# Kernel optimization log

Hardware: AMD Instinct MI355X
Metric: run time of the kernel (lower is better)

The kernel has to match this reference:

```python
import jax, jax.numpy as jnp
import numpy as np

B, S, D, UNITS = 32, 4096, 512, 512


def setup_inputs() -> dict:
    key = jax.random.key(0)
    ks = jax.random.split(key, 8)
    scale = 0.05
    return {
        "query": jax.random.normal(ks[0], (B, D), dtype=jnp.float32),
        "values": jax.random.normal(ks[1], (B, S, D), dtype=jnp.float32),
        "W1": jax.random.normal(ks[2], (D, UNITS), dtype=jnp.float32) * scale,
        "b1": jnp.zeros((UNITS,), dtype=jnp.float32),
        "W2": jax.random.normal(ks[3], (D, UNITS), dtype=jnp.float32) * scale,
        "b2": jnp.zeros((UNITS,), dtype=jnp.float32),
        "V": jax.random.normal(ks[4], (UNITS, 1), dtype=jnp.float32) * scale,
        "bv": jnp.zeros((1,), dtype=jnp.float32),
    }


def reference(query, values, W1, b1, W2, b2, V, bv):
    # values: [B, S, D], query: [B, D]
    proj_v = jnp.einsum("bsd,du->bsu", values, W1) + b1          # [B, S, U]
    proj_q = (query @ W2 + b2)[:, None, :]                        # [B, 1, U]
    score = jnp.tanh(proj_v + proj_q) @ V + bv                    # [B, S, 1]
    attention_weights = jax.nn.softmax(score, axis=1)             # [B, S, 1]
    context_vector = jnp.sum(attention_weights * values, axis=1)  # [B, D]
    return (context_vector, attention_weights)
```

## Files before the change

### kernel.cpp

```cpp
#include <hip/hip_runtime.h>

#define NB 32
#define NS 4096
#define ND 512
#define NU 512

typedef __attribute__((ext_vector_type(8))) __bf16 bf16x8;
typedef __attribute__((ext_vector_type(8))) short short8;
typedef __attribute__((ext_vector_type(4))) float f32x4;

union Cvt8 { __bf16 h[8]; short8 s8; };

__device__ __forceinline__ float fast_tanh(float x) {
  float e = __expf(2.0f * x);
  return 1.0f - __fdividef(2.0f, e + 1.0f);
}

__global__ void pack_w1_kernel(const float* __restrict__ W1, __bf16* __restrict__ W1f) {
  int idx = blockIdx.x * 256 + threadIdx.x;
  int l  = idx & 63;
  int ct = (idx >> 6) & 31;
  int ks = idx >> 11;
  int col   = ct * 16 + (l & 15);
  int kbase = ks * 32 + (l >> 4) * 8;
  Cvt8 u;
#pragma unroll
  for (int j = 0; j < 8; ++j) u.h[j] = (__bf16)W1[(size_t)(kbase + j) * NU + col];
  *reinterpret_cast<short8*>(W1f + (size_t)idx * 8) = u.s8;
}

__global__ void proj_query_kernel(const float* __restrict__ query, const float* __restrict__ W2,
                                  const float* __restrict__ b2, const float* __restrict__ b1,
                                  float* __restrict__ pq) {
  int b = blockIdx.y;
  int u = blockIdx.x * 256 + threadIdx.x;
  const float* q = query + (size_t)b * ND;
  float acc = b2[u] + b1[u];
  for (int k = 0; k < ND; ++k) acc += q[k] * W2[(size_t)k * NU + u];
  pq[(size_t)b * NU + u] = acc;
}

__global__ __launch_bounds__(512, 4)
void score_kernel(const float* __restrict__ values, const __bf16* __restrict__ W1f,
                  const float* __restrict__ pq, const float* __restrict__ V,
                  float* __restrict__ scoreW) {
  __shared__ __align__(16) char ldsb[67584];
  float* sbuf = (float*)(ldsb + 65536);

  int bid = blockIdx.x;
  int b = bid >> 6;
  int s0 = (bid & 63) * 64;
  int tid = threadIdx.x;
  int l = tid & 63;
  int w = tid >> 6;
  int lane_col = l & 15;
  int lane_k8  = l >> 4;

  float pqv[4], Vv[4];
#pragma unroll
  for (int nb = 0; nb < 2; ++nb)
#pragma unroll
    for (int cf = 0; cf < 2; ++cf) {
      int col = nb * 256 + w * 32 + cf * 16 + lane_col;
      pqv[nb * 2 + cf] = pq[(size_t)b * NU + col];
      Vv[nb * 2 + cf]  = V[col];
    }

  const float* vbase = values + ((size_t)b * NS + s0) * ND;

#pragma unroll
  for (int i = 0; i < 8; ++i) {
    int c  = i * 512 + tid;
    int t  = c >> 10;
    int kg = (c >> 6) & 15;
    int ln = c & 63;
    int s  = t * 16 + (ln & 15);
    int c8 = kg * 4 + (ln >> 4);
    const float4* p = reinterpret_cast<const float4*>(vbase + (size_t)s * ND + c8 * 8);
    float4 f0 = p[0], f1 = p[1];
    Cvt8 u;
    u.h[0] = (__bf16)f0.x; u.h[1] = (__bf16)f0.y; u.h[2] = (__bf16)f0.z; u.h[3] = (__bf16)f0.w;
    u.h[4] = (__bf16)f1.x; u.h[5] = (__bf16)f1.y; u.h[6] = (__bf16)f1.z; u.h[7] = (__bf16)f1.w;
    *reinterpret_cast<short8*>(ldsb + (size_t)c * 16) = u.s8;
  }
  __syncthreads();

  float partial[4][4];
#pragma unroll
  for (int t = 0; t < 4; ++t)
#pragma unroll
    for (int r = 0; r < 4; ++r) partial[t][r] = 0.f;

#pragma unroll
  for (int nb = 0; nb < 2; ++nb) {
    f32x4 acc[4][2];
#pragma unroll
    for (int t = 0; t < 4; ++t)
#pragma unroll
      for (int cf = 0; cf < 2; ++cf) acc[t][cf] = (f32x4){0.f, 0.f, 0.f, 0.f};

    const __bf16* wp = W1f + ((size_t)(nb * 16 + w * 2) * 64 + l) * 8;

    bf16x8 aa[2][4];
    bf16x8 bbb[2][2];
#pragma unroll
    for (int t = 0; t < 4; ++t)
      aa[0][t] = *reinterpret_cast<const bf16x8*>(ldsb + (((t * 16 + 0) * 64 + l) << 4));
#pragma unroll
    for (int cf = 0; cf < 2; ++cf)
      bbb[0][cf] = *reinterpret_cast<const bf16x8*>(wp + (size_t)0 * 16384 + cf * 512);

#pragma unroll
    for (int kg = 0; kg < 16; ++kg) {
      const int cur = kg & 1, nxt = cur ^ 1;
      if (kg < 15) {
#pragma unroll
        for (int t = 0; t < 4; ++t)
          aa[nxt][t] = *reinterpret_cast<const bf16x8*>(ldsb + (((t * 16 + kg + 1) * 64 + l) << 4));
#pragma unroll
        for (int cf = 0; cf < 2; ++cf)
          bbb[nxt][cf] = *reinterpret_cast<const bf16x8*>(wp + (size_t)(kg + 1) * 16384 + cf * 512);
      }
      __builtin_amdgcn_s_setprio(1);
#pragma unroll
      for (int cf = 0; cf < 2; ++cf)
#pragma unroll
        for (int t = 0; t < 4; ++t)
          acc[t][cf] = __builtin_amdgcn_mfma_f32_16x16x32_bf16(aa[cur][t], bbb[cur][cf], acc[t][cf], 0, 0, 0);
      __builtin_amdgcn_s_setprio(0);
    }

#pragma unroll
    for (int cf = 0; cf < 2; ++cf)
#pragma unroll
      for (int t = 0; t < 4; ++t)
#pragma unroll
        for (int r = 0; r < 4; ++r)
          partial[t][r] += fast_tanh(acc[t][cf][r] + pqv[nb * 2 + cf]) * Vv[nb * 2 + cf];
  }

#pragma unroll
  for (int off = 1; off < 16; off <<= 1)
#pragma unroll
    for (int t = 0; t < 4; ++t)
#pragma unroll
      for (int r = 0; r < 4; ++r) partial[t][r] += __shfl_xor(partial[t][r], off);

  if (lane_col == 0) {
#pragma unroll
    for (int t = 0; t < 4; ++t)
#pragma unroll
      for (int r = 0; r < 4; ++r)
        sbuf[w * 64 + t * 16 + lane_k8 * 4 + r] = partial[t][r];
  }
  __syncthreads();
  if (tid < 64) {
    float sc = 0.f;
#pragma unroll
    for (int wv = 0; wv < 8; ++wv) sc += sbuf[wv * 64 + tid];
    scoreW[(size_t)b * NS + s0 + tid] = sc;
  }
}

__global__ void softmax_kernel(const float* __restrict__ scoreW, float* __restrict__ attn) {
  int b = blockIdx.x, tid = threadIdx.x;
  __shared__ float sred[8];
  const float* sc = scoreW + (size_t)b * NS;
  float m = -3.0e38f;
  for (int s = tid; s < NS; s += 256) m = fmaxf(m, sc[s]);
#pragma unroll
  for (int off = 1; off < 64; off <<= 1) m = fmaxf(m, __shfl_xor(m, off));
  if ((tid & 63) == 0) sred[tid >> 6] = m;
  __syncthreads();
  m = fmaxf(fmaxf(sred[0], sred[1]), fmaxf(sred[2], sred[3]));
  float sum = 0.f;
  for (int s = tid; s < NS; s += 256) sum += __expf(sc[s] - m);
#pragma unroll
  for (int off = 1; off < 64; off <<= 1) sum += __shfl_xor(sum, off);
  if ((tid & 63) == 0) sred[4 + (tid >> 6)] = sum;
  __syncthreads();
  float inv = 1.f / (sred[4] + sred[5] + sred[6] + sred[7]);
  float* ab = attn + (size_t)b * NS;
  for (int s = tid; s < NS; s += 256) ab[s] = __expf(sc[s] - m) * inv;
}

__global__ void context_partial_kernel(const float* __restrict__ values,
                                       const float* __restrict__ attn,
                                       float* __restrict__ ctxpart) {
  int blk = blockIdx.x;
  int b = blk >> 4, c = blk & 15;
  int tid = threadIdx.x;
  int t2 = tid & 127;
  int sg = tid >> 7;
  const float* vb = values + ((size_t)b * NS + c * 256) * ND;
  const float* ab = attn + (size_t)b * NS + c * 256;
  f32x4 acc = {0.f, 0.f, 0.f, 0.f};
  for (int s = sg; s < 256; s += 2) {
    float wv = ab[s];
    f32x4 v = *reinterpret_cast<const f32x4*>(vb + (size_t)s * ND + t2 * 4);
    acc += v * wv;
  }
  __shared__ f32x4 red[128];
  if (sg == 1) red[t2] = acc;
  __syncthreads();
  if (sg == 0) {
    acc += red[t2];
    *reinterpret_cast<f32x4*>(ctxpart + (size_t)blk * ND + t2 * 4) = acc;
  }
}

__global__ void context_reduce_kernel(const float* __restrict__ ctxpart, float* __restrict__ ctx) {
  int b = blockIdx.x, tid = threadIdx.x;
  f32x4 acc = {0.f, 0.f, 0.f, 0.f};
  for (int c = 0; c < 16; ++c)
    acc += *reinterpret_cast<const f32x4*>(ctxpart + (size_t)(b * 16 + c) * ND + tid * 4);
  *reinterpret_cast<f32x4*>(ctx + (size_t)b * ND + tid * 4) = acc;
}

extern "C" void kernel_launch(void* const* d_in, const int* in_sizes, int n_in,
                              void* d_out, int out_size, void* d_ws, size_t ws_size,
                              hipStream_t stream) {
  const float* query  = (const float*)d_in[0];
  const float* values = (const float*)d_in[1];
  const float* W1     = (const float*)d_in[2];
  const float* b1     = (const float*)d_in[3];
  const float* W2     = (const float*)d_in[4];
  const float* b2     = (const float*)d_in[5];
  const float* V      = (const float*)d_in[6];

  float* ctx_out  = (float*)d_out;
  float* attn_out = ctx_out + NB * ND;

  char* ws = (char*)d_ws;
  __bf16* W1f    = (__bf16*)ws;
  float*  pq     = (float*)(ws + 524288);
  float*  scoreW = (float*)(ws + 589824);
  float*  ctxp   = (float*)(ws + 1114112);

  hipLaunchKernelGGL(pack_w1_kernel,        dim3(128),     dim3(256), 0, stream, W1, W1f);
  hipLaunchKernelGGL(proj_query_kernel,     dim3(2, NB),   dim3(256), 0, stream, query, W2, b2, b1, pq);
  hipLaunchKernelGGL(score_kernel,          dim3(2048),    dim3(512), 0, stream, values, W1f, pq, V, scoreW);
  hipLaunchKernelGGL(softmax_kernel,        dim3(NB),      dim3(256), 0, stream, scoreW, attn_out);
  hipLaunchKernelGGL(context_partial_kernel,dim3(NB * 16), dim3(256), 0, stream, values, attn_out, ctxp);
  hipLaunchKernelGGL(context_reduce_kernel, dim3(NB),      dim3(128), 0, stream, ctxp, ctx_out);
}
```

Measured before the change: 197.0 us.

## Enlarge score tile to 128 rows, overlap second-half staging with MFMA

Each score-kernel block now covers 128 sequence rows instead of 64, with waves split into 4 column groups times 2 row halves. Each wave computes a 64x64 output patch, so every W1 fragment loaded from global memory feeds twice as many MFMAs. The second half of the values tile is loaded and converted to bf16 inside the first 8 k-steps of the first column pass, overlapping global loads with matrix math, and block IDs are swizzled across XCDs. The cost is 130 KB of LDS per block, lower occupancy (launch bounds 2), more accumulator registers, and the s_setprio hints are removed.

```diff
diff --git a/kernel.cpp b/kernel.cpp
--- a/kernel.cpp
+++ b/kernel.cpp
@@ -40,48 +40,62 @@
   pq[(size_t)b * NU + u] = acc;
 }
 
-__global__ __launch_bounds__(512, 4)
+__global__ __launch_bounds__(512, 2)
 void score_kernel(const float* __restrict__ values, const __bf16* __restrict__ W1f,
                   const float* __restrict__ pq, const float* __restrict__ V,
                   float* __restrict__ scoreW) {
-  __shared__ __align__(16) char ldsb[67584];
-  float* sbuf = (float*)(ldsb + 65536);
-
-  int bid = blockIdx.x;
-  int b = bid >> 6;
-  int s0 = (bid & 63) * 64;
+  __shared__ __align__(16) char ldsb[133120];
+  float* sbuf = (float*)(ldsb + 131072);
+
+  int bid0 = blockIdx.x;
+  int bid = (bid0 & 7) * 128 + (bid0 >> 3);
+  int b = bid >> 5;
+  int s0 = (bid & 31) * 128;
   int tid = threadIdx.x;
   int l = tid & 63;
   int w = tid >> 6;
   int lane_col = l & 15;
   int lane_k8  = l >> 4;
-
-  float pqv[4], Vv[4];
+  int cq = w & 3;
+  int h  = w >> 2;
+
+  float pqv[8], Vv[8];
 #pragma unroll
   for (int nb = 0; nb < 2; ++nb)
 #pragma unroll
-    for (int cf = 0; cf < 2; ++cf) {
-      int col = nb * 256 + w * 32 + cf * 16 + lane_col;
-      pqv[nb * 2 + cf] = pq[(size_t)b * NU + col];
-      Vv[nb * 2 + cf]  = V[col];
+    for (int cf = 0; cf < 4; ++cf) {
+      int col = nb * 256 + cq * 64 + cf * 16 + lane_col;
+      pqv[nb * 4 + cf] = pq[(size_t)b * NU + col];
+      Vv[nb * 4 + cf]  = V[col];
     }
 
   const float* vbase = values + ((size_t)b * NS + s0) * ND;
 
-#pragma unroll
-  for (int i = 0; i < 8; ++i) {
-    int c  = i * 512 + tid;
-    int t  = c >> 10;
-    int kg = (c >> 6) & 15;
-    int ln = c & 63;
-    int s  = t * 16 + (ln & 15);
+  auto stage_load = [&](f32x4* s, int i) {
+    int c = i * 512 + tid;
+    int tg = c >> 10, kg = (c >> 6) & 15, ln = c & 63;
+    int srow = tg * 16 + (ln & 15);
     int c8 = kg * 4 + (ln >> 4);
-    const float4* p = reinterpret_cast<const float4*>(vbase + (size_t)s * ND + c8 * 8);
-    float4 f0 = p[0], f1 = p[1];
+    const f32x4* p = reinterpret_cast<const f32x4*>(vbase + (size_t)srow * ND + c8 * 8);
+    s[0] = p[0]; s[1] = p[1];
+  };
+  auto stage_write = [&](const f32x4* s, int i) {
+    int c = i * 512 + tid;
     Cvt8 u;
-    u.h[0] = (__bf16)f0.x; u.h[1] = (__bf16)f0.y; u.h[2] = (__bf16)f0.z; u.h[3] = (__bf16)f0.w;
-    u.h[4] = (__bf16)f1.x; u.h[5] = (__bf16)f1.y; u.h[6] = (__bf16)f1.z; u.h[7] = (__bf16)f1.w;
+    u.h[0] = (__bf16)s[0].x; u.h[1] = (__bf16)s[0].y; u.h[2] = (__bf16)s[0].z; u.h[3] = (__bf16)s[0].w;
+    u.h[4] = (__bf16)s[1].x; u.h[5] = (__bf16)s[1].y; u.h[6] = (__bf16)s[1].z; u.h[7] = (__bf16)s[1].w;
     *reinterpret_cast<short8*>(ldsb + (size_t)c * 16) = u.s8;
+  };
+
+  {
+    f32x4 sA[2], sB[2];
+#pragma unroll
+    for (int ii = 0; ii < 4; ++ii) {
+      stage_load(sA, ii * 4);
+      stage_load(sB, ii * 4 + 2);
+      stage_write(sA, ii * 4);
+      stage_write(sB, ii * 4 + 2);
+    }
   }
   __syncthreads();
 
@@ -91,52 +105,90 @@
 #pragma unroll
     for (int r = 0; r < 4; ++r) partial[t][r] = 0.f;
 
-#pragma unroll
-  for (int nb = 0; nb < 2; ++nb) {
-    f32x4 acc[4][2];
-#pragma unroll
-    for (int t = 0; t < 4; ++t)
-#pragma unroll
-      for (int cf = 0; cf < 2; ++cf) acc[t][cf] = (f32x4){0.f, 0.f, 0.f, 0.f};
-
-    const __bf16* wp = W1f + ((size_t)(nb * 16 + w * 2) * 64 + l) * 8;
-
-    bf16x8 aa[2][4];
-    bf16x8 bbb[2][2];
-#pragma unroll
-    for (int t = 0; t < 4; ++t)
-      aa[0][t] = *reinterpret_cast<const bf16x8*>(ldsb + (((t * 16 + 0) * 64 + l) << 4));
-#pragma unroll
-    for (int cf = 0; cf < 2; ++cf)
-      bbb[0][cf] = *reinterpret_cast<const bf16x8*>(wp + (size_t)0 * 16384 + cf * 512);
-
+  const int tgb = h * 4;
+
+  {
+    f32x4 acc[4][4];
+#pragma unroll
+    for (int t = 0; t < 4; ++t)
+#pragma unroll
+      for (int cf = 0; cf < 4; ++cf) acc[t][cf] = (f32x4){0.f, 0.f, 0.f, 0.f};
+
+    const __bf16* wp = W1f + ((size_t)(cq * 4) * 64 + l) * 8;
+    bf16x8 bbb[2][4];
+#pragma unroll
+    for (int cf = 0; cf < 4; ++cf)
+      bbb[0][cf] = *reinterpret_cast<const bf16x8*>(wp + (size_t)(cf) * 512);
+
+    f32x4 stp[2][2];
 #pragma unroll
     for (int kg = 0; kg < 16; ++kg) {
       const int cur = kg & 1, nxt = cur ^ 1;
+      if (kg >= 1 && kg <= 8) stage_write(stp[(kg - 1) & 1], 2 * (kg - 1) + 1);
+      if (kg == 8) __syncthreads();
+      if (kg < 8) stage_load(stp[kg & 1], 2 * kg + 1);
+      bf16x8 a[4];
+#pragma unroll
+      for (int t = 0; t < 4; ++t)
+        a[t] = *reinterpret_cast<const bf16x8*>(ldsb + ((((tgb + t) * 16 + kg) * 64 + l) << 4));
       if (kg < 15) {
 #pragma unroll
-        for (int t = 0; t < 4; ++t)
-          aa[nxt][t] = *reinterpret_cast<const bf16x8*>(ldsb + (((t * 16 + kg + 1) * 64 + l) << 4));
-#pragma unroll
-        for (int cf = 0; cf < 2; ++cf)
+        for (int cf = 0; cf < 4; ++cf)
           bbb[nxt][cf] = *reinterpret_cast<const bf16x8*>(wp + (size_t)(kg + 1) * 16384 + cf * 512);
       }
-      __builtin_amdgcn_s_setprio(1);
-#pragma unroll
-      for (int cf = 0; cf < 2; ++cf)
+#pragma unroll
+      for (int cf = 0; cf < 4; ++cf)
 #pragma unroll
         for (int t = 0; t < 4; ++t)
-          acc[t][cf] = __builtin_amdgcn_mfma_f32_16x16x32_bf16(aa[cur][t], bbb[cur][cf], acc[t][cf], 0, 0, 0);
-      __builtin_amdgcn_s_setprio(0);
-    }
-
-#pragma unroll
-    for (int cf = 0; cf < 2; ++cf)
+          acc[t][cf] = __builtin_amdgcn_mfma_f32_16x16x32_bf16(a[t], bbb[cur][cf], acc[t][cf], 0, 0, 0);
+    }
+#pragma unroll
+    for (int cf = 0; cf < 4; ++cf)
 #pragma unroll
       for (int t = 0; t < 4; ++t)
 #pragma unroll
         for (int r = 0; r < 4; ++r)
-          partial[t][r] += fast_tanh(acc[t][cf][r] + pqv[nb * 2 + cf]) * Vv[nb * 2 + cf];
+          partial[t][r] += fast_tanh(acc[t][cf][r] + pqv[cf]) * Vv[cf];
+  }
+
+  {
+    f32x4 acc[4][4];
+#pragma unroll
+    for (int t = 0; t < 4; ++t)
+#pragma unroll
+      for (int cf = 0; cf < 4; ++cf) acc[t][cf] = (f32x4){0.f, 0.f, 0.f, 0.f};
+
+    const __bf16* wp = W1f + ((size_t)(16 + cq * 4) * 64 + l) * 8;
+    bf16x8 bbb[2][4];
+#pragma unroll
+    for (int cf = 0; cf < 4; ++cf)
+      bbb[0][cf] = *reinterpret_cast<const bf16x8*>(wp + (size_t)(cf) * 512);
+
+#pragma unroll
+    for (int kg = 0; kg < 16; ++kg) {
+      const int cur = kg & 1, nxt = cur ^ 1;
+      bf16x8 a[4];
+#pragma unroll
+      for (int t = 0; t < 4; ++t)
+        a[t] = *reinterpret_cast<const bf16x8*>(ldsb + ((((tgb + t) * 16 + kg) * 64 + l) << 4));
+      if (kg < 15) {
+#pragma unroll
+        for (int cf = 0; cf < 4; ++cf)
+          bbb[nxt][cf] = *reinterpret_cast<const bf16x8*>(wp + (size_t)(kg + 1) * 16384 + cf * 512);
+      }
+#pragma unroll
+      for (int cf = 0; cf < 4; ++cf)
+#pragma unroll
+        for (int t = 0; t < 4; ++t)
+          acc[t][cf] = __builtin_amdgcn_mfma_f32_16x16x32_bf16(a[t], bbb[cur][cf], acc[t][cf], 0, 0, 0);
+    }
+#pragma unroll
+    for (int cf = 0; cf < 4; ++cf)
+#pragma unroll
+      for (int t = 0; t < 4; ++t)
+#pragma unroll
+        for (int r = 0; r < 4; ++r)
+          partial[t][r] += fast_tanh(acc[t][cf][r] + pqv[4 + cf]) * Vv[4 + cf];
   }
 
 #pragma unroll
@@ -154,10 +206,11 @@
         sbuf[w * 64 + t * 16 + lane_k8 * 4 + r] = partial[t][r];
   }
   __syncthreads();
-  if (tid < 64) {
+  if (tid < 128) {
+    int hh = tid >> 6, loc = tid & 63;
     float sc = 0.f;
 #pragma unroll
-    for (int wv = 0; wv < 8; ++wv) sc += sbuf[wv * 64 + tid];
+    for (int q = 0; q < 4; ++q) sc += sbuf[(hh * 4 + q) * 64 + loc];
     scoreW[(size_t)b * NS + s0 + tid] = sc;
   }
 }
@@ -239,7 +292,7 @@
 
   hipLaunchKernelGGL(pack_w1_kernel,        dim3(128),     dim3(256), 0, stream, W1, W1f);
   hipLaunchKernelGGL(proj_query_kernel,     dim3(2, NB),   dim3(256), 0, stream, query, W2, b2, b1, pq);
-  hipLaunchKernelGGL(score_kernel,          dim3(2048),    dim3(512), 0, stream, values, W1f, pq, V, scoreW);
+  hipLaunchKernelGGL(score_kernel,          dim3(1024),    dim3(512), 0, stream, values, W1f, pq, V, scoreW);
   hipLaunchKernelGGL(softmax_kernel,        dim3(NB),      dim3(256), 0, stream, scoreW, attn_out);
   hipLaunchKernelGGL(context_partial_kernel,dim3(NB * 16), dim3(256), 0, stream, values, attn_out, ctxp);
   hipLaunchKernelGGL(context_reduce_kernel, dim3(NB),      dim3(128), 0, stream, ctxp, ctx_out);
```

Result: slower. 285.6 us (+45.0%).
